# Optimization experiments

Hardware: AMD Instinct MI355X
Metric: run time of the kernel (lower is better)

Reference implementation:

```python
import jax, jax.numpy as jnp
import numpy as np

B, T, D_MODEL, D_STATE = 8, 2048, 1024, 256


def setup_inputs() -> dict:
    key = jax.random.key(0)
    ks = jax.random.split(key, 11)
    def lecun(k, shape):
        fan_in = shape[0]
        return jax.random.normal(k, shape, jnp.float32) / jnp.sqrt(jnp.float32(fan_in))
    return {
        "x": jax.random.normal(ks[0], (B, T, D_MODEL), jnp.float32),
        "W_in": lecun(ks[1], (D_MODEL, D_STATE)),
        "b_in": jnp.zeros((D_STATE,), jnp.float32),
        "W_gate": lecun(ks[2], (D_MODEL, D_MODEL)),
        "b_gate": jnp.zeros((D_MODEL,), jnp.float32),
        "A": lecun(ks[3], (D_STATE, D_STATE)),
        "Bm": lecun(ks[4], (D_STATE, D_STATE)),
        "C": lecun(ks[5], (D_MODEL, D_STATE)),
        "D": lecun(ks[6], (D_MODEL, D_STATE)),
        "W_out": lecun(ks[7], (D_MODEL, D_MODEL)),
        "b_out": jnp.zeros((D_MODEL,), jnp.float32),
    }


def reference(x, W_in, b_in, W_gate, b_gate, A, Bm, C, D, W_out, b_out):
    b, t, d_model = x.shape
    d_state = A.shape[0]
    u = x @ W_in + b_in                      # [B,T,d_state]
    g = jax.nn.sigmoid(x @ W_gate + b_gate)  # [B,T,d_model]

    u_seq = jnp.swapaxes(u, 0, 1)  # [T,B,d_state]
    g_seq = jnp.swapaxes(g, 0, 1)  # [T,B,d_model]
    x_seq = jnp.swapaxes(x, 0, 1)  # [T,B,d_model]

    def step(h_prev, inputs):
        u_t, g_t, x_t = inputs
        h_t = jnp.tanh(h_prev @ A + u_t @ Bm)            # [B,d_state]
        y_t = h_t @ C.T + u_t @ D.T                      # [B,d_model]
        y_t = g_t * y_t + (1.0 - g_t) * x_t
        return h_t, y_t

    h0 = jnp.zeros((b, d_state), x.dtype)
    _, ys = jax.lax.scan(step, h0, xs=(u_seq, g_seq, x_seq))
    ys = jnp.swapaxes(ys, 0, 1)  # [B,T,d_model]
    return ys @ W_out + b_out + x
```

## Files before the change

### kernel.cpp

```cpp
#include <hip/hip_runtime.h>
#include <math.h>


enum { E_NONE = 0, E_BIASBF = 1, E_SIGBF = 2, E_GATE = 3, E_BIASRES = 4, E_CVTBF = 5 };

typedef __attribute__((ext_vector_type(8))) short bf16x8;
typedef __attribute__((ext_vector_type(4))) float f32x4;

static __device__ inline unsigned short f2bf(float f) {
    unsigned u = __builtin_bit_cast(unsigned, f);
    unsigned r = (u + 0x7fff + ((u >> 16) & 1)) >> 16;
    return (unsigned short)r;
}
static __device__ inline unsigned pack2(float a, float b) {
    return (unsigned)f2bf(a) | ((unsigned)f2bf(b) << 16);
}
static __device__ inline float bflo(unsigned u) {
    return __builtin_bit_cast(float, u << 16);
}
static __device__ inline float bfhi(unsigned u) {
    return __builtin_bit_cast(float, u & 0xffff0000u);
}
static __device__ inline float tanh_fast(float x) {
    float e = __builtin_amdgcn_exp2f(x * 2.8853900817779268f);
    float t = __builtin_amdgcn_rcpf(e + 1.0f);
    return fmaf(-2.0f, t, 1.0f);
}

static __device__ __forceinline__ void cvt_body(
    const float* __restrict__ in, unsigned short* __restrict__ out, int i, int n8)
{
    if (i >= n8) return;
    float4 a = ((const float4*)in)[i * 2];
    float4 b = ((const float4*)in)[i * 2 + 1];
    uint4 o;
    o.x = pack2(a.x, a.y); o.y = pack2(a.z, a.w);
    o.z = pack2(b.x, b.y); o.w = pack2(b.z, b.w);
    ((uint4*)out)[i] = o;
}

__global__ __launch_bounds__(256) void cvt_bf(
    const float* __restrict__ in, unsigned short* __restrict__ out, int n8)
{
    cvt_body(in, out, blockIdx.x * 256 + threadIdx.x, n8);
}

static __device__ __forceinline__ void transpose_tile(
    bool act, unsigned char* LdsB, int bxi, int byi, int t2,
    const float* __restrict__ in, unsigned short* __restrict__ out, int R, int C)
{
    float* tile = (float*)LdsB;
    const int bx = bxi * 32, by = byi * 32;
    const int tx = t2 & 31, ty = t2 >> 5;
    if (act) {
#pragma unroll
        for (int i = 0; i < 32; i += 8)
            tile[(ty + i) * 33 + tx] = in[(size_t)(by + ty + i) * C + bx + tx];
    }
    __syncthreads();
    if (act) {
#pragma unroll
        for (int i = 0; i < 32; i += 8)
            out[(size_t)(bx + ty + i) * R + by + tx] = f2bf(tile[tx * 33 + ty + i]);
    }
}

__global__ __launch_bounds__(256) void transpose_bf(
    const float* __restrict__ in, unsigned short* __restrict__ out, int R, int C)
{
    __shared__ __align__(16) unsigned char Lds[32 * 33 * 4];
    transpose_tile(true, Lds, blockIdx.x, blockIdx.y, threadIdx.x, in, out, R, C);
}

template <int EPI>
static __device__ __forceinline__ void gemm_tile(
    bool act, unsigned char* Lds, int bx, int by, int tid,
    const unsigned short* __restrict__ Ag,
    const unsigned short* __restrict__ Bg,
    const float* __restrict__ bias, const float* __restrict__ res,
    const float* __restrict__ acc_src, const unsigned short* __restrict__ g8,
    void* Cg, int M, int N, int K)
{
    const int w = (tid >> 6) & 3, l = tid & 63;
    const int r = l & 15, g = l >> 4;
    const int m0 = by * 128, n0 = bx * 128;

    const unsigned char* agp[4];
    const unsigned char* bgp[4];
#pragma unroll
    for (int j = 0; j < 4; ++j) {
        const int c = w * 256 + j * 64 + l;
        const int row = c >> 3;
        const unsigned offp = ((unsigned)(c & 7) * 16u) ^ ((unsigned)(row & 7) * 16u);
        agp[j] = (const unsigned char*)Ag + ((size_t)(m0 + row) * K) * 2 + offp;
        bgp[j] = (const unsigned char*)Bg + ((size_t)(n0 + row) * K) * 2 + offp;
    }

#define GSTAGE(BUF)                                                           \
    {                                                                         \
      _Pragma("unroll")                                                       \
      for (int j = 0; j < 4; ++j) {                                           \
        __builtin_amdgcn_global_load_lds(                                     \
            (const __attribute__((address_space(1))) unsigned*)(agp[j]),      \
            (__attribute__((address_space(3))) unsigned*)(Lds + (BUF) * 32768 + w * 4096 + j * 1024), \
            16, 0, 0);                                                        \
        __builtin_amdgcn_global_load_lds(                                     \
            (const __attribute__((address_space(1))) unsigned*)(bgp[j]),      \
            (__attribute__((address_space(3))) unsigned*)(Lds + (BUF) * 32768 + 16384 + w * 4096 + j * 1024), \
            16, 0, 0);                                                        \
        agp[j] += 128; bgp[j] += 128;                                         \
      }                                                                       \
    }

    f32x4 acc[2][8];
#pragma unroll
    for (int mt = 0; mt < 2; ++mt)
#pragma unroll
        for (int nt = 0; nt < 8; ++nt) acc[mt][nt] = (f32x4){0.f, 0.f, 0.f, 0.f};

    const int nk = K >> 6;
    if (act) GSTAGE(0)
    __syncthreads();
    for (int t = 0; t < nk; ++t) {
        const int buf = t & 1;
        if (act) {
            if (t + 1 < nk) GSTAGE(buf ^ 1)
            bf16x8 af[2][2], bfr[8][2];
#pragma unroll
            for (int s = 0; s < 2; ++s) {
#pragma unroll
                for (int mt = 0; mt < 2; ++mt) {
                    const int row = w * 32 + mt * 16 + r;
                    af[mt][s] = *(const bf16x8*)(Lds + buf * 32768 + row * 128 +
                        ((s * 64 + 16 * g) ^ (16 * (row & 7))));
                }
#pragma unroll
                for (int nt = 0; nt < 8; ++nt) {
                    const int row = nt * 16 + r;
                    bfr[nt][s] = *(const bf16x8*)(Lds + buf * 32768 + 16384 + row * 128 +
                        ((s * 64 + 16 * g) ^ (16 * (row & 7))));
                }
            }
#pragma unroll
            for (int s = 0; s < 2; ++s)
#pragma unroll
                for (int mt = 0; mt < 2; ++mt)
#pragma unroll
                    for (int nt = 0; nt < 8; ++nt)
                        acc[mt][nt] = __builtin_amdgcn_mfma_f32_16x16x32_bf16(
                            af[mt][s], bfr[nt][s], acc[mt][nt], 0, 0, 0);
        }
        __syncthreads();
    }
#undef GSTAGE

    if (act) {
#pragma unroll
        for (int mt = 0; mt < 2; ++mt)
#pragma unroll
            for (int nt = 0; nt < 8; ++nt) {
                const int n = n0 + nt * 16 + r;
                float bv = 0.f;
                if (EPI == E_BIASBF || EPI == E_SIGBF || EPI == E_BIASRES) bv = bias[n];
#pragma unroll
                for (int q = 0; q < 4; ++q) {
                    const int m = m0 + w * 32 + mt * 16 + g * 4 + q;
                    const size_t idx = (size_t)m * N + n;
                    float v = acc[mt][nt][q] + bv;
                    if (EPI == E_SIGBF) v = 1.f / (1.f + expf(-v));
                    if (EPI == E_BIASRES) v += res[idx];
                    if (EPI == E_GATE) {
                        v += acc_src[idx];
                        const float gg = bflo((unsigned)g8[idx]);
                        v = gg * v + (1.f - gg) * res[idx];
                    }
                    if (EPI == E_BIASBF || EPI == E_SIGBF || EPI == E_CVTBF ||
                        EPI == E_GATE)
                        ((unsigned short*)Cg)[idx] = f2bf(v);
                    else
                        ((float*)Cg)[idx] = v;
                }
            }
    }
}

template <int EPI>
__global__ __launch_bounds__(256) void gemm_mfma(
    const unsigned short* __restrict__ Ag, const unsigned short* __restrict__ Bg,
    const float* __restrict__ bias, const float* __restrict__ res,
    const float* __restrict__ acc_src, const unsigned short* __restrict__ g8,
    void* Cg, int M, int N, int K)
{
    __shared__ __align__(16) unsigned char Lds[65536];
    gemm_tile<EPI>(true, Lds, blockIdx.x, blockIdx.y, threadIdx.x,
                   Ag, Bg, bias, res, acc_src, g8, Cg, M, N, K);
}

static __device__ __forceinline__ void scan_body(
    unsigned char* LDSM, int tid,
    const float* __restrict__ Amat, const unsigned short* __restrict__ u2bf,
    unsigned short* __restrict__ hbf)
{
    constexpr int T = 2048;
    constexpr int NCH = T / 8;
    unsigned char* Hb = LDSM;
    unsigned char* Ub = LDSM + 65536;

    const int w = tid >> 6, l = tid & 63;
    const int r = l & 15, g = l >> 4, r8 = r & 7;
    const bool hi = (r & 8) != 0;
    const int m0 = w * 32;

    ((unsigned*)Hb)[tid] = 0u;
    ((unsigned*)Hb)[tid + 512] = 0u;

    bf16x8 af[2][8];
#pragma unroll
    for (int mt = 0; mt < 2; ++mt) {
        const int m = m0 + mt * 16 + r;
#pragma unroll
        for (int kt = 0; kt < 8; ++kt) {
            unsigned wd[4];
#pragma unroll
            for (int jw = 0; jw < 4; ++jw) {
                const int k = kt * 32 + g * 8 + jw * 2;
                wd[jw] = pack2(Amat[(size_t)k * 256 + m],
                               Amat[(size_t)(k + 1) * 256 + m]);
            }
            af[mt][kt] = __builtin_bit_cast(bf16x8, *(uint4*)wd);
        }
    }

    unsigned ubase[2], woff[2];
#pragma unroll
    for (int mt = 0; mt < 2; ++mt) {
        const int s0 = m0 + mt * 16 + g * 4;
        const int s = s0 + (hi ? 2 : 0);
        ubase[mt] = (unsigned)(r8 * 512 + (((s >> 3) ^ r8) * 16) + (s & 7) * 2);
        woff[mt] = (unsigned)((((s0 >> 5) * 32 + ((s0 >> 3) & 3) * 8 + r8) * 16)
                              + ((s0 & 7) + (hi ? 2 : 0)) * 2);
    }
    const unsigned rbase = (unsigned)((g * 8 + r8) * 16);

    int sg_i[4], sg_b[4], sg_kg[4];
#pragma unroll
    for (int j = 0; j < 4; ++j) {
        const int d = j * 512 + tid;
        sg_i[j] = d >> 8;
        sg_b[j] = (d >> 5) & 7;
        sg_kg[j] = (d & 31) ^ sg_b[j];
    }

#pragma unroll
    for (int c0 = 0; c0 < 2; ++c0)
#pragma unroll
        for (int j = 0; j < 4; ++j) {
            const size_t srcb = ((size_t)(sg_b[j] * T + c0 * 8 + sg_i[j]) * 512)
                              + (unsigned)(sg_kg[j] * 16);
            __builtin_amdgcn_global_load_lds(
                (const __attribute__((address_space(1))) unsigned*)(
                    (const unsigned char*)u2bf + srcb),
                (__attribute__((address_space(3))) unsigned*)(
                    Ub + c0 * 32768 + (j * 512 + tid) * 16), 16, 0, 0);
        }
    asm volatile("s_waitcnt vmcnt(0) lgkmcnt(0)" ::: "memory");
    __builtin_amdgcn_sched_barrier(0);
    __builtin_amdgcn_s_barrier();
    __builtin_amdgcn_sched_barrier(0);

#define SCAN_STEP(I)                                                          \
  {                                                                           \
    const unsigned sr = ((unsigned)(t0 + (I)) & 15u) * 4096u;                 \
    const unsigned sw = ((unsigned)(t0 + (I) + 1) & 15u) * 4096u;             \
    bf16x8 hf[8];                                                             \
    _Pragma("unroll")                                                         \
    for (int kt = 0; kt < 8; ++kt)                                            \
      hf[kt] = *(const bf16x8*)(Hb + sr + rbase + (unsigned)(kt * 512));      \
    unsigned uv[2];                                                           \
    _Pragma("unroll")                                                         \
    for (int mt = 0; mt < 2; ++mt)                                            \
      uv[mt] = *(const unsigned*)(Uc + (unsigned)(I) * 4096u + ubase[mt]);    \
    f32x4 p0[2], p1[2];                                                       \
    _Pragma("unroll")                                                         \
    for (int mt = 0; mt < 2; ++mt) {                                          \
      p0[mt] = (f32x4){0.f, 0.f, 0.f, 0.f};                                   \
      p1[mt] = (f32x4){0.f, 0.f, 0.f, 0.f};                                   \
    }                                                                         \
    _Pragma("unroll")                                                         \
    for (int kt = 0; kt < 4; ++kt) {                                          \
      _Pragma("unroll")                                                       \
      for (int mt = 0; mt < 2; ++mt) {                                        \
        p0[mt] = __builtin_amdgcn_mfma_f32_16x16x32_bf16(af[mt][kt], hf[kt],  \
                                                         p0[mt], 0, 0, 0);    \
        p1[mt] = __builtin_amdgcn_mfma_f32_16x16x32_bf16(                     \
            af[mt][kt + 4], hf[kt + 4], p1[mt], 0, 0, 0);                     \
      }                                                                       \
    }                                                                         \
    _Pragma("unroll")                                                         \
    for (int mt = 0; mt < 2; ++mt) {                                          \
      const float slo = hi ? (p0[mt][2] + p1[mt][2]) : (p0[mt][0] + p1[mt][0]);\
      const float shi = hi ? (p0[mt][3] + p1[mt][3]) : (p0[mt][1] + p1[mt][1]);\
      const float h0 = tanh_fast(slo + bflo(uv[mt]));                         \
      const float h1 = tanh_fast(shi + bfhi(uv[mt]));                         \
      unsigned pk;                                                            \
      asm("v_cvt_pk_bf16_f32 %0, %1, %2" : "=v"(pk) : "v"(h0), "v"(h1));      \
      *(unsigned*)(Hb + sw + woff[mt]) = pk;                                  \
    }                                                                         \
    asm volatile("s_waitcnt lgkmcnt(0)" ::: "memory");                        \
    __builtin_amdgcn_sched_barrier(0);                                        \
    __builtin_amdgcn_s_barrier();                                             \
    __builtin_amdgcn_sched_barrier(0);                                        \
  }

    for (int chunk = 0; chunk < NCH; ++chunk) {
        const int t0 = chunk * 8;
        const unsigned char* Uc = Ub + ((unsigned)(chunk & 1) << 15);

        SCAN_STEP(0)
        SCAN_STEP(1)
        SCAN_STEP(2)
        SCAN_STEP(3)
        SCAN_STEP(4)
        SCAN_STEP(5)
        SCAN_STEP(6)
        SCAN_STEP(7)

        {
#pragma unroll
            for (int j = 0; j < 4; ++j) {
                const int p = j * 512 + tid;
                const int di = p >> 8, wp = p & 255;
                const int kt_ = wp >> 5, sl_ = wp & 31;
                const unsigned slot = (unsigned)((t0 + 1 + di) & 15) * 4096u;
                uint4 dat = *(const uint4*)(Hb + slot + (unsigned)wp * 16u);
                const size_t off = ((size_t)((sl_ & 7) * T + t0 + di) * 256 +
                                    kt_ * 32 + (sl_ >> 3) * 8);
                *(uint4*)(hbf + off) = dat;
            }
            if (chunk + 2 < NCH) {
                const unsigned nb = (unsigned)(chunk & 1) << 15;
#pragma unroll
                for (int j = 0; j < 4; ++j) {
                    const size_t srcb =
                        ((size_t)(sg_b[j] * T + t0 + 16 + sg_i[j]) * 512)
                        + (unsigned)(sg_kg[j] * 16);
                    __builtin_amdgcn_global_load_lds(
                        (const __attribute__((address_space(1))) unsigned*)(
                            (const unsigned char*)u2bf + srcb),
                        (__attribute__((address_space(3))) unsigned*)(
                            Ub + nb + (j * 512 + tid) * 16), 16, 0, 0);
                }
                asm volatile("s_waitcnt vmcnt(8) lgkmcnt(0)" ::: "memory");
            } else {
                asm volatile("s_waitcnt vmcnt(4) lgkmcnt(0)" ::: "memory");
            }
            __builtin_amdgcn_sched_barrier(0);
            __builtin_amdgcn_s_barrier();
            __builtin_amdgcn_sched_barrier(0);
        }
    }
#undef SCAN_STEP
}

__global__ __launch_bounds__(512, 1) void fused_scan(
    const float* __restrict__ Amat, const unsigned short* __restrict__ u2bf,
    unsigned short* __restrict__ hbf,
    const unsigned short* __restrict__ xbf, const unsigned short* __restrict__ WgT,
    const float* __restrict__ b_gate, unsigned short* __restrict__ gbf,
    const unsigned short* __restrict__ u, const unsigned short* __restrict__ Dbf,
    float* __restrict__ big,
    const float* __restrict__ W_out, unsigned short* __restrict__ WoT,
    const float* __restrict__ Cm, unsigned short* __restrict__ Cbf,
    int M, int DM, int DS)
{
    __shared__ __align__(16) unsigned char LDSM[131072];
    const int tid = threadIdx.x;
    const unsigned bid = blockIdx.x;

    if (bid == 0) {
        scan_body(LDSM, tid, Amat, u2bf, hbf);
        return;
    }
    const bool act = tid < 256;
    const int t2 = tid & 255;
    if (bid <= 1024) {
        const int t = bid - 1;
        gemm_tile<E_SIGBF>(act, LDSM, t & 7, t >> 3, t2, xbf, WgT, b_gate,
                           nullptr, nullptr, nullptr, gbf, M, DM, DM);
    } else if (bid <= 2048) {
        const int t = bid - 1025;
        gemm_tile<E_NONE>(act, LDSM, t & 7, t >> 3, t2, u, Dbf, nullptr,
                          nullptr, nullptr, nullptr, big, M, DM, DS);
    } else if (bid <= 3072) {
        const int t = bid - 2049;
        transpose_tile(act, LDSM, t & 31, t >> 5, t2, W_out, WoT, DM, DM);
    } else {
        const int t = bid - 3073;
        if (act) cvt_body(Cm, Cbf, t * 256 + t2, DM * DS / 8);
    }
}

extern "C" void kernel_launch(void* const* d_in, const int* in_sizes, int n_in,
                              void* d_out, int out_size, void* d_ws, size_t ws_size,
                              hipStream_t stream)
{
    const float* x      = (const float*)d_in[0];
    const float* W_in   = (const float*)d_in[1];
    const float* b_in   = (const float*)d_in[2];
    const float* W_gate = (const float*)d_in[3];
    const float* b_gate = (const float*)d_in[4];
    const float* Amat   = (const float*)d_in[5];
    const float* Bm     = (const float*)d_in[6];
    const float* Cm     = (const float*)d_in[7];
    const float* Dm     = (const float*)d_in[8];
    const float* W_out  = (const float*)d_in[9];
    const float* b_out  = (const float*)d_in[10];

    const int T = 2048, DM = 1024, DS = 256;
    const int M = 8 * T;
    const size_t MB = 1024 * 1024;
    char* ws = (char*)d_ws;

    unsigned short* xbf  = (unsigned short*)(ws);
    unsigned short* ysbf = xbf;
    unsigned short* u    = (unsigned short*)(ws + 32 * MB);
    unsigned short* u2   = (unsigned short*)(ws + 40 * MB);
    unsigned short* h    = (unsigned short*)(ws + 56 * MB);
    unsigned short* WinT = (unsigned short*)(ws + 64 * MB);
    unsigned short* BmT  = (unsigned short*)(ws + 64 * MB + 512 * 1024);
    unsigned short* WgT  = (unsigned short*)(ws + 65 * MB);
    unsigned short* WoT  = (unsigned short*)(ws + 67 * MB);
    unsigned short* Cbf  = (unsigned short*)(ws + 69 * MB);
    unsigned short* Dbf  = (unsigned short*)(ws + 69 * MB + 512 * 1024);
    float*          big  = (float*)(ws + 70 * MB);
    unsigned short* gbf  = (unsigned short*)(ws + 134 * MB);

    cvt_bf<<<M * DM / 8 / 256, 256, 0, stream>>>(x, xbf, M * DM / 8);
    transpose_bf<<<dim3(DS / 32, DM / 32), 256, 0, stream>>>(W_in, WinT, DM, DS);
    transpose_bf<<<dim3(DS / 32, DS / 32), 256, 0, stream>>>(Bm, BmT, DS, DS);
    transpose_bf<<<dim3(DM / 32, DM / 32), 256, 0, stream>>>(W_gate, WgT, DM, DM);
    cvt_bf<<<DM * DS / 8 / 256, 256, 0, stream>>>(Dm, Dbf, DM * DS / 8);

    gemm_mfma<E_BIASBF><<<dim3(DS / 128, M / 128), 256, 0, stream>>>(
        xbf, WinT, b_in, nullptr, nullptr, nullptr, u, M, DS, DM);
    gemm_mfma<E_CVTBF><<<dim3(DS / 128, M / 128), 256, 0, stream>>>(
        u, BmT, nullptr, nullptr, nullptr, nullptr, u2, M, DS, DS);

    fused_scan<<<3201, 512, 0, stream>>>(
        Amat, u2, h, xbf, WgT, b_gate, gbf, u, Dbf, big, W_out, WoT, Cm, Cbf,
        M, DM, DS);

    gemm_mfma<E_GATE><<<dim3(DM / 128, M / 128), 256, 0, stream>>>(
        h, Cbf, nullptr, x, big, gbf, ysbf, M, DM, DS);
    gemm_mfma<E_BIASRES><<<dim3(DM / 128, M / 128), 256, 0, stream>>>(
        ysbf, WoT, b_out, x, nullptr, nullptr, (float*)d_out, M, DM, DM);
}
```

Baseline: 1.445 ms.

## Fold input projection into Bm and D weights, fuse prep kernels

Precomputes the combined weights W_in·Bm and W_in·D^T, plus the matching biases, so that u2 and the D-term both come straight from x. This drops the intermediate u GEMM and the u2 = u·Bm GEMM. The cost is that the D-term GEMM inside fused_scan now has K=1024 instead of 256, which adds work running in parallel with the scan. The five prep launches are also merged into a single prep_all kernel.

```diff
diff --git a/kernel.cpp b/kernel.cpp
--- a/kernel.cpp
+++ b/kernel.cpp
@@ -2,7 +2,8 @@
 #include <math.h>
 
 
-enum { E_NONE = 0, E_BIASBF = 1, E_SIGBF = 2, E_GATE = 3, E_BIASRES = 4, E_CVTBF = 5 };
+enum { E_NONE = 0, E_BIASBF = 1, E_SIGBF = 2, E_GATE = 3, E_BIASRES = 4,
+       E_CVTBF = 5, E_BIASF32 = 6 };
 
 typedef __attribute__((ext_vector_type(8))) short bf16x8;
 typedef __attribute__((ext_vector_type(4))) float f32x4;
@@ -39,12 +40,6 @@
     ((uint4*)out)[i] = o;
 }
 
-__global__ __launch_bounds__(256) void cvt_bf(
-    const float* __restrict__ in, unsigned short* __restrict__ out, int n8)
-{
-    cvt_body(in, out, blockIdx.x * 256 + threadIdx.x, n8);
-}
-
 static __device__ __forceinline__ void transpose_tile(
     bool act, unsigned char* LdsB, int bxi, int byi, int t2,
     const float* __restrict__ in, unsigned short* __restrict__ out, int R, int C)
@@ -65,11 +60,39 @@
     }
 }
 
-__global__ __launch_bounds__(256) void transpose_bf(
-    const float* __restrict__ in, unsigned short* __restrict__ out, int R, int C)
+__global__ __launch_bounds__(256) void prep_all(
+    const float* __restrict__ x, unsigned short* __restrict__ xbf,
+    const float* __restrict__ W_in, unsigned short* __restrict__ Winbf,
+    const float* __restrict__ Dm, unsigned short* __restrict__ Dbf,
+    const float* __restrict__ Bm, unsigned short* __restrict__ BmT,
+    const float* __restrict__ W_gate, unsigned short* __restrict__ WgT,
+    const float* __restrict__ b_in, float* __restrict__ b2, float* __restrict__ bD)
 {
     __shared__ __align__(16) unsigned char Lds[32 * 33 * 4];
-    transpose_tile(true, Lds, blockIdx.x, blockIdx.y, threadIdx.x, in, out, R, C);
+    const unsigned bid = blockIdx.x;
+    const int tid = threadIdx.x;
+    if (bid < 8192) {
+        cvt_body(x, xbf, bid * 256 + tid, 16384 * 1024 / 8);
+    } else if (bid < 8320) {
+        cvt_body(W_in, Winbf, (bid - 8192) * 256 + tid, 1024 * 256 / 8);
+    } else if (bid < 8448) {
+        cvt_body(Dm, Dbf, (bid - 8320) * 256 + tid, 1024 * 256 / 8);
+    } else if (bid < 8512) {
+        const int t = bid - 8448;
+        transpose_tile(true, Lds, t & 7, t >> 3, tid, Bm, BmT, 256, 256);
+    } else if (bid < 9536) {
+        const int t = bid - 8512;
+        transpose_tile(true, Lds, t & 31, t >> 5, tid, W_gate, WgT, 1024, 1024);
+    } else if (bid == 9536) {
+        float s = 0.f;
+        for (int k = 0; k < 256; ++k) s = fmaf(b_in[k], Bm[k * 256 + tid], s);
+        b2[tid] = s;
+    } else {
+        const int n = (bid - 9537) * 256 + tid;
+        float s = 0.f;
+        for (int k = 0; k < 256; ++k) s = fmaf(b_in[k], Dm[n * 256 + k], s);
+        bD[n] = s;
+    }
 }
 
 template <int EPI>
@@ -161,7 +184,8 @@
             for (int nt = 0; nt < 8; ++nt) {
                 const int n = n0 + nt * 16 + r;
                 float bv = 0.f;
-                if (EPI == E_BIASBF || EPI == E_SIGBF || EPI == E_BIASRES) bv = bias[n];
+                if (EPI == E_BIASBF || EPI == E_SIGBF || EPI == E_BIASRES ||
+                    EPI == E_BIASF32) bv = bias[n];
 #pragma unroll
                 for (int q = 0; q < 4; ++q) {
                     const int m = m0 + w * 32 + mt * 16 + g * 4 + q;
@@ -367,7 +391,7 @@
     unsigned short* __restrict__ hbf,
     const unsigned short* __restrict__ xbf, const unsigned short* __restrict__ WgT,
     const float* __restrict__ b_gate, unsigned short* __restrict__ gbf,
-    const unsigned short* __restrict__ u, const unsigned short* __restrict__ Dbf,
+    const unsigned short* __restrict__ WDT, const float* __restrict__ bD,
     float* __restrict__ big,
     const float* __restrict__ W_out, unsigned short* __restrict__ WoT,
     const float* __restrict__ Cm, unsigned short* __restrict__ Cbf,
@@ -389,8 +413,8 @@
                            nullptr, nullptr, nullptr, gbf, M, DM, DM);
     } else if (bid <= 2048) {
         const int t = bid - 1025;
-        gemm_tile<E_NONE>(act, LDSM, t & 7, t >> 3, t2, u, Dbf, nullptr,
-                          nullptr, nullptr, nullptr, big, M, DM, DS);
+        gemm_tile<E_BIASF32>(act, LDSM, t & 7, t >> 3, t2, xbf, WDT, bD,
+                             nullptr, nullptr, nullptr, big, M, DM, DM);
     } else if (bid <= 3072) {
         const int t = bid - 2049;
         transpose_tile(act, LDSM, t & 31, t >> 5, t2, W_out, WoT, DM, DM);
@@ -421,33 +445,36 @@
     const size_t MB = 1024 * 1024;
     char* ws = (char*)d_ws;
 
-    unsigned short* xbf  = (unsigned short*)(ws);
-    unsigned short* ysbf = xbf;
-    unsigned short* u    = (unsigned short*)(ws + 32 * MB);
-    unsigned short* u2   = (unsigned short*)(ws + 40 * MB);
-    unsigned short* h    = (unsigned short*)(ws + 56 * MB);
-    unsigned short* WinT = (unsigned short*)(ws + 64 * MB);
-    unsigned short* BmT  = (unsigned short*)(ws + 64 * MB + 512 * 1024);
-    unsigned short* WgT  = (unsigned short*)(ws + 65 * MB);
-    unsigned short* WoT  = (unsigned short*)(ws + 67 * MB);
-    unsigned short* Cbf  = (unsigned short*)(ws + 69 * MB);
-    unsigned short* Dbf  = (unsigned short*)(ws + 69 * MB + 512 * 1024);
-    float*          big  = (float*)(ws + 70 * MB);
-    unsigned short* gbf  = (unsigned short*)(ws + 134 * MB);
-
-    cvt_bf<<<M * DM / 8 / 256, 256, 0, stream>>>(x, xbf, M * DM / 8);
-    transpose_bf<<<dim3(DS / 32, DM / 32), 256, 0, stream>>>(W_in, WinT, DM, DS);
-    transpose_bf<<<dim3(DS / 32, DS / 32), 256, 0, stream>>>(Bm, BmT, DS, DS);
-    transpose_bf<<<dim3(DM / 32, DM / 32), 256, 0, stream>>>(W_gate, WgT, DM, DM);
-    cvt_bf<<<DM * DS / 8 / 256, 256, 0, stream>>>(Dm, Dbf, DM * DS / 8);
+    unsigned short* xbf   = (unsigned short*)(ws);
+    unsigned short* ysbf  = xbf;
+    unsigned short* Winbf = (unsigned short*)(ws + 32 * MB);
+    unsigned short* Dbf   = (unsigned short*)(ws + 33 * MB);
+    unsigned short* W2T   = (unsigned short*)(ws + 34 * MB);
+    unsigned short* WDT   = (unsigned short*)(ws + 35 * MB);
+    float*          b2    = (float*)(ws + 38 * MB);
+    float*          bD    = (float*)(ws + 38 * MB + 65536);
+    unsigned short* u2    = (unsigned short*)(ws + 40 * MB);
+    unsigned short* h     = (unsigned short*)(ws + 56 * MB);
+    unsigned short* BmT   = (unsigned short*)(ws + 64 * MB);
+    unsigned short* WgT   = (unsigned short*)(ws + 65 * MB);
+    unsigned short* WoT   = (unsigned short*)(ws + 67 * MB);
+    unsigned short* Cbf   = (unsigned short*)(ws + 69 * MB);
+    float*          big   = (float*)(ws + 70 * MB);
+    unsigned short* gbf   = (unsigned short*)(ws + 134 * MB);
+
+    prep_all<<<9541, 256, 0, stream>>>(x, xbf, W_in, Winbf, Dm, Dbf, Bm, BmT,
+                                       W_gate, WgT, b_in, b2, bD);
+
+    gemm_mfma<E_CVTBF><<<dim3(DM / 128, DS / 128), 256, 0, stream>>>(
+        BmT, Winbf, nullptr, nullptr, nullptr, nullptr, W2T, DS, DM, DS);
+    gemm_mfma<E_CVTBF><<<dim3(DM / 128, DM / 128), 256, 0, stream>>>(
+        Dbf, Winbf, nullptr, nullptr, nullptr, nullptr, WDT, DM, DM, DS);
 
     gemm_mfma<E_BIASBF><<<dim3(DS / 128, M / 128), 256, 0, stream>>>(
-        xbf, WinT, b_in, nullptr, nullptr, nullptr, u, M, DS, DM);
-    gemm_mfma<E_CVTBF><<<dim3(DS / 128, M / 128), 256, 0, stream>>>(
-        u, BmT, nullptr, nullptr, nullptr, nullptr, u2, M, DS, DS);
+        xbf, W2T, b2, nullptr, nullptr, nullptr, u2, M, DS, DM);
 
     fused_scan<<<3201, 512, 0, stream>>>(
-        Amat, u2, h, xbf, WgT, b_gate, gbf, u, Dbf, big, W_out, WoT, Cm, Cbf,
+        Amat, u2, h, xbf, WgT, b_gate, gbf, WDT, bD, big, W_out, WoT, Cm, Cbf,
         M, DM, DS);
 
     gemm_mfma<E_GATE><<<dim3(DM / 128, M / 128), 256, 0, stream>>>(
```

New measurement: 1.453 ms. Within noise of the previous version (+0.6%).
